# Kernel optimization log

Hardware: AMD Instinct MI355X
Metric: run time of the kernel (lower is better)

The kernel has to match this reference:

```python
import jax, jax.numpy as jnp
import numpy as np
from functools import partial

NUM_HEADS = 8
EPS = 1e-12  # torch F.normalize default eps


def conv1x1(x, w):
    # x: [b,i,h,w], w: [o,i] -> [b,o,h,w]
    return jnp.einsum('oi,bihw->bohw', w, x)


def dwconv3x3(x, w):
    # depthwise 3x3, SAME padding; x: [b,c,h,w], w: [c,1,3,3]
    c = x.shape[1]
    return jax.lax.conv_general_dilated(
        x, w, window_strides=(1, 1), padding='SAME',
        dimension_numbers=('NCHW', 'OIHW', 'NCHW'), feature_group_count=c)


def setup_inputs() -> dict:
    key = jax.random.key(0)
    ks = jax.random.split(key, 16)
    b, dim, h, w = 2, 128, 256, 256
    d8 = dim // 8
    f = lambda k, shape, fan: (jax.random.normal(k, shape, jnp.float32) * (1.0 / np.sqrt(fan)))
    return {
        'x': jax.random.normal(ks[0], (b, dim, h, w), jnp.float32),
        'y': jax.random.normal(ks[1], (b, dim, h, w), jnp.float32),
        'qkv_w': f(ks[2], (dim * 3, dim), dim),
        'qkv_dw_w': f(ks[3], (dim * 3, 1, 3, 3), 9),
        'proj_w': f(ks[4], (dim, dim), dim),
        'sa_w1': f(ks[5], (d8, dim), dim),
        'sa_w2': f(ks[6], (d8, d8), d8),
        'sa_w3': f(ks[7], (1, d8), d8),
        'sp_w1': f(ks[8], (d8, dim), dim),
        'sp_w2': f(ks[9], (d8, d8), d8),
        'sp_w3': f(ks[10], (dim, d8), d8),
        'dw_w': f(ks[11], (dim, 1, 3, 3), 9),
        'temperature': jnp.ones((NUM_HEADS, 1, 1), jnp.float32),
    }


def reference(x, y, qkv_w, qkv_dw_w, proj_w, sa_w1, sa_w2, sa_w3,
              sp_w1, sp_w2, sp_w3, dw_w, temperature):
    b, c, h, w = x.shape
    hd = NUM_HEADS
    # QKV: 1x1 conv then depthwise 3x3
    qkv = dwconv3x3(conv1x1(x, qkv_w), qkv_dw_w)
    q, k, v = jnp.split(qkv, 3, axis=1)
    # Spatial attention gate from y: [b,1,h,w]
    sa = jax.nn.sigmoid(conv1x1(jax.nn.relu(conv1x1(jax.nn.relu(conv1x1(y, sa_w1)), sa_w2)), sa_w3))
    q = q * sa
    # b (head c) h w -> b head c (h w)
    shp = (b, hd, c // hd, h * w)
    q = q.reshape(shp)
    k = k.reshape(shp)
    v = v.reshape(shp)
    # L2 normalize along spatial axis (torch F.normalize semantics)
    q = q / jnp.maximum(jnp.linalg.norm(q, axis=-1, keepdims=True), EPS)
    k = k / jnp.maximum(jnp.linalg.norm(k, axis=-1, keepdims=True), EPS)
    # channel-wise attention: [b,head,c/head,c/head]
    attn = jnp.einsum('bhcn,bhdn->bhcd', q, k) * temperature
    attn = jax.nn.softmax(attn, axis=-1)
    out = jnp.einsum('bhcd,bhdn->bhcn', attn, v).reshape(b, c, h, w)
    # Spectral attention gate from out: [b,c]
    pooled = jnp.mean(out, axis=(2, 3))
    g = jax.nn.gelu(pooled @ sp_w1.T, approximate=False)
    g = jax.nn.gelu(g @ sp_w2.T, approximate=False)
    spec = jax.nn.sigmoid(g @ sp_w3.T)[:, :, None, None]
    y2 = dwconv3x3(y, dw_w) * spec
    return conv1x1(out + y2, proj_w)
```

## Files before the change

kernel.cpp:

```cpp
#include <hip/hip_runtime.h>
#include <hip/hip_bf16.h>

typedef __hip_bfloat16 bf16;
typedef __attribute__((ext_vector_type(8))) short short8;
typedef __attribute__((ext_vector_type(4))) short short4v;
typedef __attribute__((ext_vector_type(4))) int   int4v;
typedef __attribute__((ext_vector_type(4))) float float4v;

#define B_   2
#define C_   128
#define H_   256
#define W_   256
#define HW_  65536
#define HD_  8
#define CH_  16
#define C3_  384
#define NG_  48

static __device__ __forceinline__ float b2f(bf16 v) { return __bfloat162float(v); }
static __device__ __forceinline__ bf16  f2b(float v) { return __float2bfloat16(v); }
static __device__ __forceinline__ short b2s(bf16 v) { return *reinterpret_cast<short*>(&v); }
static __device__ __forceinline__ float su2f(short s) {
  return __uint_as_float(((unsigned)(unsigned short)s) << 16);
}
static __device__ __forceinline__ short f2s(float v) { bf16 h = f2b(v); return b2s(h); }
static __device__ __forceinline__ short8 smask(short8 v, int m) {
  int4v iv = *(int4v*)&v;
  iv = iv & m;
  return *(short8*)&iv;
}

__global__ void k_wprep(const float* __restrict__ qkv_w, const float* __restrict__ proj_w,
                        const float* __restrict__ sa_w1,
                        float* __restrict__ wt_qkvT, float* __restrict__ wt_proj,
                        float* __restrict__ wt_sa1, bf16* __restrict__ wt_qkv_bf,
                        bf16* __restrict__ wt_proj_bf, int do_bf) {
  int idx = blockIdx.x * 256 + threadIdx.x;
  if (idx < C3_ * C_) { int o = idx / C_, i = idx % C_; wt_qkvT[i * C3_ + o] = qkv_w[idx]; }
  if (idx < C_ * C_)  { int o = idx / C_, i = idx % C_; wt_proj[i * C_ + o] = proj_w[idx]; }
  if (idx < 16 * C_)  { int j = idx / C_, i = idx % C_; wt_sa1[i * 16 + j] = sa_w1[idx]; }
  if (do_bf && idx < C3_ * C_) {
    int o = idx / C_, k = idx % C_;
    int sk = ((((k >> 3) ^ (o & 7)) << 3) | (k & 7));
    wt_qkv_bf[o * C_ + sk] = f2b(qkv_w[idx]);
  }
  if (do_bf && idx < C_ * C_) {
    int o = idx / C_, k = idx % C_;
    int sk = ((((k >> 3) ^ (o & 7)) << 3) | (k & 7));
    wt_proj_bf[o * C_ + sk] = f2b(proj_w[idx]);
  }
}

__global__ void __launch_bounds__(256) k_sa(
    const float* __restrict__ y, const float* __restrict__ wt_sa1,
    const float* __restrict__ sa_w2, const float* __restrict__ sa_w3,
    float* __restrict__ sa) {
  int b = blockIdx.y;
  int p0 = (blockIdx.x * 256 + threadIdx.x) * 2;
  const float* yp = y + (size_t)b * C_ * HW_ + p0;
  float t1a[16], t1b[16];
#pragma unroll
  for (int j = 0; j < 16; ++j) { t1a[j] = 0.f; t1b[j] = 0.f; }
  for (int i = 0; i < C_; ++i) {
    float2 v = *(const float2*)(yp + (size_t)i * HW_);
    const float* wr = wt_sa1 + i * 16;
#pragma unroll
    for (int j = 0; j < 16; ++j) { t1a[j] = fmaf(wr[j], v.x, t1a[j]); t1b[j] = fmaf(wr[j], v.y, t1b[j]); }
  }
#pragma unroll
  for (int j = 0; j < 16; ++j) { t1a[j] = fmaxf(t1a[j], 0.f); t1b[j] = fmaxf(t1b[j], 0.f); }
  float t2a[16], t2b[16];
#pragma unroll
  for (int j = 0; j < 16; ++j) {
    float sx = 0.f, sy = 0.f;
#pragma unroll
    for (int l = 0; l < 16; ++l) { float w = sa_w2[j * 16 + l]; sx = fmaf(w, t1a[l], sx); sy = fmaf(w, t1b[l], sy); }
    t2a[j] = fmaxf(sx, 0.f); t2b[j] = fmaxf(sy, 0.f);
  }
  float sa3 = 0.f, sb3 = 0.f;
#pragma unroll
  for (int j = 0; j < 16; ++j) { float w = sa_w3[j]; sa3 = fmaf(w, t2a[j], sa3); sb3 = fmaf(w, t2b[j], sb3); }
  sa[(size_t)b * HW_ + p0]     = 1.f / (1.f + expf(-sa3));
  sa[(size_t)b * HW_ + p0 + 1] = 1.f / (1.f + expf(-sb3));
}

__global__ void __launch_bounds__(256) k_convm(
    const float* __restrict__ x, const bf16* __restrict__ wbf, bf16* __restrict__ pre) {
  __shared__ bf16 XT[2][64][128];
  __shared__ bf16 AT[128][128];
  int b = blockIdx.y;
  int p0 = blockIdx.x * 64;
  int t = threadIdx.x;

  {
    int p  = t & 63;
    int c0 = t >> 6;
    const float* xp = x + (size_t)b * C_ * HW_ + p0 + p;
#pragma unroll
    for (int it = 0; it < 4; ++it) {
      int c = c0 + it * 4;
      short8 hv, lv;
#pragma unroll
      for (int j = 0; j < 8; ++j) {
        float v = xp[(size_t)(c * 8 + j) * HW_];
        bf16 h = f2b(v);
        bf16 l = f2b(v - b2f(h));
        hv[j] = b2s(h); lv[j] = b2s(l);
      }
      int sc = c ^ (p & 7);
      *(short8*)&XT[0][p][sc * 8] = hv;
      *(short8*)&XT[1][p][sc * 8] = lv;
    }
  }

  int lane = t & 63, wave = t >> 6;
  int m = lane & 15, quad = lane >> 4;
  int wr = wave >> 1, wc = wave & 1;
  float4v acc[4][2];

  for (int mb = 0; mb < 3; ++mb) {
    __syncthreads();
    {
      const short8* src = (const short8*)(wbf + mb * C_ * C_);
      short8* dst = (short8*)&AT[0][0];
#pragma unroll
      for (int j = 0; j < 8; ++j)
        dst[j * 256 + t] = src[j * 256 + t];
    }
    __syncthreads();

#pragma unroll
    for (int mt = 0; mt < 4; ++mt)
#pragma unroll
      for (int nt = 0; nt < 2; ++nt)
#pragma unroll
        for (int e = 0; e < 4; ++e) acc[mt][nt][e] = 0.f;

#pragma unroll
    for (int kk = 0; kk < 4; ++kk) {
      int cidx = (((kk * 4 + quad) ^ (m & 7)) << 3);
      short8 af[4], bh[2], bl[2];
#pragma unroll
      for (int mt = 0; mt < 4; ++mt)
        af[mt] = *(const short8*)&AT[wr * 64 + mt * 16 + m][cidx];
#pragma unroll
      for (int nt = 0; nt < 2; ++nt) {
        bh[nt] = *(const short8*)&XT[0][wc * 32 + nt * 16 + m][cidx];
        bl[nt] = *(const short8*)&XT[1][wc * 32 + nt * 16 + m][cidx];
      }
#pragma unroll
      for (int mt = 0; mt < 4; ++mt)
#pragma unroll
        for (int nt = 0; nt < 2; ++nt) {
          acc[mt][nt] = __builtin_amdgcn_mfma_f32_16x16x32_bf16(af[mt], bh[nt], acc[mt][nt], 0, 0, 0);
          acc[mt][nt] = __builtin_amdgcn_mfma_f32_16x16x32_bf16(af[mt], bl[nt], acc[mt][nt], 0, 0, 0);
        }
    }

#pragma unroll
    for (int mt = 0; mt < 4; ++mt)
#pragma unroll
      for (int nt = 0; nt < 2; ++nt) {
        int gl = mb * 16 + wr * 8 + mt * 2 + (quad >> 1);
        int p = wc * 32 + nt * 16 + m;
        short4v sv;
#pragma unroll
        for (int reg = 0; reg < 4; ++reg) sv[reg] = f2s(acc[mt][nt][reg]);
        bf16* dp = pre + (((size_t)b * NG_ + gl) * HW_ + p0 + p) * 8 + (quad & 1) * 4;
        *(short4v*)dp = sv;
      }
  }
}

__global__ void __launch_bounds__(256) k_dwgram(
    const bf16* __restrict__ pre, const float* __restrict__ dww,
    const float* __restrict__ sa, float* __restrict__ attn_raw,
    float* __restrict__ ssq_q, float* __restrict__ ssq_k) {
  __shared__ char smem[65536];
  bf16 (*dwb)[256] = (bf16 (*)[256])(smem + 49152);
  float* red = (float*)smem;

  int b = blockIdx.z, head = blockIdx.y, r0 = blockIdx.x * 8;
  int t = threadIdx.x;
  const float* saw = sa + (size_t)b * HW_;

  int g0 = head * 2;
  size_t gbase0 = (((size_t)b * NG_ + g0)      * HW_) * 8;
  size_t gbase1 = (((size_t)b * NG_ + g0 + 1)  * HW_) * 8;
  size_t gbase2 = (((size_t)b * NG_ + 16 + g0) * HW_) * 8;
  size_t gbase3 = (((size_t)b * NG_ + 17 + g0) * HW_) * 8;

  auto loadrow = [&](int r, int soff) {
    if (r < 0 || r >= H_) {
      short8 z = {0, 0, 0, 0, 0, 0, 0, 0};
      *(short8*)(smem + soff + 0 * 4096 + t * 16) = z;
      *(short8*)(smem + soff + 1 * 4096 + t * 16) = z;
      *(short8*)(smem + soff + 2 * 4096 + t * 16) = z;
      *(short8*)(smem + soff + 3 * 4096 + t * 16) = z;
      return;
    }
    size_t poff = ((size_t)(r * W_ + t)) * 8;
    *(short8*)(smem + soff + 0 * 4096 + t * 16) = *(const short8*)(pre + gbase0 + poff);
    *(short8*)(smem + soff + 1 * 4096 + t * 16) = *(const short8*)(pre + gbase1 + poff);
    *(short8*)(smem + soff + 2 * 4096 + t * 16) = *(const short8*)(pre + gbase2 + poff);
    *(short8*)(smem + soff + 3 * 4096 + t * 16) = *(const short8*)(pre + gbase3 + poff);
  };

  loadrow(r0 - 1, 0); loadrow(r0, 16384); loadrow(r0 + 1, 32768);
  __syncthreads();

  int lane = t & 63, wave = t >> 6;
  int m = lane & 15, quad = lane >> 4;
  int sch = t >> 3;
  int colL = ((t > 0) ? (t - 1) : 0) * 16;
  int colC = t * 16;
  int colR = ((t < W_ - 1) ? (t + 1) : (W_ - 1)) * 16;
  int mskl = (t > 0) ? -1 : 0;
  int mskr = (t < W_ - 1) ? -1 : 0;
  float4v acc = {0.f, 0.f, 0.f, 0.f};
  float sacc = 0.f;

  int so0 = 0, so1 = 16384, so2 = 32768;

  for (int i = 0; i < 8; ++i) {
    int rr = r0 + i;
    short8 q0v, q1v, q2v, q3v;
    bool pf = (i < 7);
    {
      short8 z = {0, 0, 0, 0, 0, 0, 0, 0};
      q0v = z; q1v = z; q2v = z; q3v = z;
    }
    if (pf && (rr + 2) < H_) {
      size_t poff = ((size_t)((rr + 2) * W_ + t)) * 8;
      q0v = *(const short8*)(pre + gbase0 + poff);
      q1v = *(const short8*)(pre + gbase1 + poff);
      q2v = *(const short8*)(pre + gbase2 + poff);
      q3v = *(const short8*)(pre + gbase3 + poff);
    }
    float gate = saw[rr * W_ + t];

    float a[32];
#pragma unroll
    for (int c = 0; c < 32; ++c) a[c] = 0.f;
#pragma unroll
    for (int dy = 0; dy < 3; ++dy) {
      int soff = (dy == 0) ? so0 : ((dy == 1) ? so1 : so2);
#pragma unroll
      for (int cg = 0; cg < 4; ++cg) {
        const char* base = smem + soff + cg * 4096;
        short8 vl = smask(*(const short8*)(base + colL), mskl);
        short8 vc = *(const short8*)(base + colC);
        short8 vr = smask(*(const short8*)(base + colR), mskr);
#pragma unroll
        for (int j = 0; j < 8; ++j) {
          int c = cg * 8 + j;
          int och = (c < 16) ? (head * CH_ + c) : (C_ + head * CH_ + c - 16);
          const float* wp = dww + och * 9 + dy * 3;
          a[c] = fmaf(wp[0], su2f(vl[j]), a[c]);
          a[c] = fmaf(wp[1], su2f(vc[j]), a[c]);
          a[c] = fmaf(wp[2], su2f(vr[j]), a[c]);
        }
      }
    }
#pragma unroll
    for (int c = 0; c < 16; ++c) a[c] *= gate;
#pragma unroll
    for (int c = 0; c < 32; ++c) dwb[c][t ^ ((c & 7) << 3)] = f2b(a[c]);
    __syncthreads();
    if (pf) {
      *(short8*)(smem + so0 + 0 * 4096 + t * 16) = q0v;
      *(short8*)(smem + so0 + 1 * 4096 + t * 16) = q1v;
      *(short8*)(smem + so0 + 2 * 4096 + t * 16) = q2v;
      *(short8*)(smem + so0 + 3 * 4096 + t * 16) = q3v;
    }
#pragma unroll
    for (int cn = 0; cn < 2; ++cn) {
      int p0 = wave * 64 + cn * 32;
      int ca = ((((p0 >> 3) + quad) ^ (m & 7)) << 3);
      short8 af = *(const short8*)&dwb[m][ca];
      short8 bfv = *(const short8*)&dwb[16 + m][ca];
      acc = __builtin_amdgcn_mfma_f32_16x16x32_bf16(af, bfv, acc, 0, 0, 0);
    }
#pragma unroll
    for (int it = 0; it < 4; ++it) {
      int c = (t & 7) + it * 8;
      int cs = c ^ (sch & 7);
      short8 v = *(const short8*)&dwb[sch][cs * 8];
#pragma unroll
      for (int j = 0; j < 8; ++j) { float f = su2f(v[j]); sacc = fmaf(f, f, sacc); }
    }
    __syncthreads();
    int tmp = so0; so0 = so1; so1 = so2; so2 = tmp;
  }

  float* ar = attn_raw + ((size_t)b * HD_ + head) * 256;
#pragma unroll
  for (int reg = 0; reg < 4; ++reg)
    atomicAdd(&ar[(quad * 4 + reg) * 16 + m], acc[reg]);
  red[t] = sacc;
  __syncthreads();
  if (t < 32) {
    float s = 0.f;
#pragma unroll
    for (int k = 0; k < 8; ++k) s += red[t * 8 + k];
    if (t < 16) atomicAdd(&ssq_q[((size_t)b * HD_ + head) * CH_ + t], s);
    else        atomicAdd(&ssq_k[((size_t)b * HD_ + head) * CH_ + t - 16], s);
  }
}

__global__ void k_softmax(const float* __restrict__ attn_raw, const float* __restrict__ ssq_q,
                          const float* __restrict__ ssq_k, const float* __restrict__ temperature,
                          float* __restrict__ attn) {
  int row = threadIdx.x;
  int bh = row >> 4;
  int head = bh & 7;
  float temp = temperature[head];
  float nq = fmaxf(sqrtf(ssq_q[row]), 1e-12f);
  float v[16];
#pragma unroll
  for (int d = 0; d < 16; ++d) {
    float nk = fmaxf(sqrtf(ssq_k[bh * 16 + d]), 1e-12f);
    v[d] = attn_raw[row * 16 + d] / (nq * nk) * temp;
  }
  float m = -1e30f;
#pragma unroll
  for (int d = 0; d < 16; ++d) m = fmaxf(m, v[d]);
  float s = 0.f;
#pragma unroll
  for (int d = 0; d < 16; ++d) { v[d] = expf(v[d] - m); s += v[d]; }
  float inv = 1.f / s;
#pragma unroll
  for (int d = 0; d < 16; ++d) attn[row * 16 + d] = v[d] * inv;
}

__global__ void __launch_bounds__(256) k_out(
    const bf16* __restrict__ pre, const float* __restrict__ dww,
    const float* __restrict__ attn, float* __restrict__ outb,
    float* __restrict__ pooled) {
  __shared__ char smem[24576];
  int b = blockIdx.z, head = blockIdx.y, r0 = blockIdx.x * 4;
  int t = threadIdx.x;

  size_t gbase0 = (((size_t)b * NG_ + 32 + head * 2)     * HW_) * 8;
  size_t gbase1 = (((size_t)b * NG_ + 32 + head * 2 + 1) * HW_) * 8;

  auto loadrow = [&](int r, int soff) {
    if (r < 0 || r >= H_) {
      short8 z = {0, 0, 0, 0, 0, 0, 0, 0};
      *(short8*)(smem + soff + 0 * 4096 + t * 16) = z;
      *(short8*)(smem + soff + 1 * 4096 + t * 16) = z;
      return;
    }
    size_t poff = ((size_t)(r * W_ + t)) * 8;
    *(short8*)(smem + soff + 0 * 4096 + t * 16) = *(const short8*)(pre + gbase0 + poff);
    *(short8*)(smem + soff + 1 * 4096 + t * 16) = *(const short8*)(pre + gbase1 + poff);
  };

  loadrow(r0 - 1, 0); loadrow(r0, 8192); loadrow(r0 + 1, 16384);
  __syncthreads();

  const float* ap = attn + ((size_t)b * HD_ + head) * 256;
  int colL = ((t > 0) ? (t - 1) : 0) * 16;
  int colC = t * 16;
  int colR = ((t < W_ - 1) ? (t + 1) : (W_ - 1)) * 16;
  int mskl = (t > 0) ? -1 : 0;
  int mskr = (t < W_ - 1) ? -1 : 0;
  float psum[16];
#pragma unroll
  for (int c = 0; c < 16; ++c) psum[c] = 0.f;

  int so0 = 0, so1 = 8192, so2 = 16384;

  for (int i = 0; i < 4; ++i) {
    int rr = r0 + i;
    short8 q0v, q1v;
    bool pf = (i < 3);
    {
      short8 z = {0, 0, 0, 0, 0, 0, 0, 0};
      q0v = z; q1v = z;
    }
    if (pf && (rr + 2) < H_) {
      size_t poff = ((size_t)((rr + 2) * W_ + t)) * 8;
      q0v = *(const short8*)(pre + gbase0 + poff);
      q1v = *(const short8*)(pre + gbase1 + poff);
    }

    float vv[16];
#pragma unroll
    for (int c = 0; c < 16; ++c) vv[c] = 0.f;
#pragma unroll
    for (int dy = 0; dy < 3; ++dy) {
      int soff = (dy == 0) ? so0 : ((dy == 1) ? so1 : so2);
#pragma unroll
      for (int cg = 0; cg < 2; ++cg) {
        const char* base = smem + soff + cg * 4096;
        short8 vl = smask(*(const short8*)(base + colL), mskl);
        short8 vc = *(const short8*)(base + colC);
        short8 vr = smask(*(const short8*)(base + colR), mskr);
#pragma unroll
        for (int j = 0; j < 8; ++j) {
          int c = cg * 8 + j;
          const float* wp = dww + (2 * C_ + head * CH_ + c) * 9 + dy * 3;
          vv[c] = fmaf(wp[0], su2f(vl[j]), vv[c]);
          vv[c] = fmaf(wp[1], su2f(vc[j]), vv[c]);
          vv[c] = fmaf(wp[2], su2f(vr[j]), vv[c]);
        }
      }
    }
    float* op = outb + ((size_t)b * C_ + head * CH_) * (size_t)HW_ + rr * W_ + t;
#pragma unroll
    for (int c2 = 0; c2 < 16; ++c2) {
      float s2 = 0.f;
#pragma unroll
      for (int d = 0; d < 16; ++d) s2 = fmaf(ap[c2 * 16 + d], vv[d], s2);
      op[(size_t)c2 * HW_] = s2;
      psum[c2] += s2;
    }
    __syncthreads();
    if (pf) {
      *(short8*)(smem + so0 + 0 * 4096 + t * 16) = q0v;
      *(short8*)(smem + so0 + 1 * 4096 + t * 16) = q1v;
    }
    __syncthreads();
    int tmp = so0; so0 = so1; so1 = so2; so2 = tmp;
  }

  int lane = t & 63;
#pragma unroll
  for (int c = 0; c < 16; ++c) {
#pragma unroll
    for (int off = 32; off > 0; off >>= 1)
      psum[c] += __shfl_xor(psum[c], off, 64);
  }
  if (lane == 0) {
    float* pp = pooled + (size_t)b * C_ + head * CH_;
#pragma unroll
    for (int c = 0; c < 16; ++c) atomicAdd(&pp[c], psum[c]);
  }
}

__global__ void k_pool(const float* __restrict__ outb, float* __restrict__ pooled) {
  int ch = blockIdx.x, b = blockIdx.y;
  const float* p = outb + ((size_t)b * C_ + ch) * (size_t)HW_;
  float s = 0.f;
  for (int i = threadIdx.x * 4; i < HW_; i += 1024) {
    float4 v = *(const float4*)(p + i);
    s += v.x + v.y + v.z + v.w;
  }
#pragma unroll
  for (int off = 32; off > 0; off >>= 1) s += __shfl_down(s, off);
  __shared__ float wsum[4];
  int lane = threadIdx.x & 63, wv = threadIdx.x >> 6;
  if (lane == 0) wsum[wv] = s;
  __syncthreads();
  if (threadIdx.x == 0) {
    float tt = wsum[0] + wsum[1] + wsum[2] + wsum[3];
    pooled[b * C_ + ch] = tt * (1.f / HW_);
  }
}

__global__ void k_spec(const float* __restrict__ pooled, const float* __restrict__ sp_w1,
                       const float* __restrict__ sp_w2, const float* __restrict__ sp_w3,
                       float* __restrict__ spec, float pscale) {
  __shared__ float g1[2][16], g2[2][16];
  int tid = threadIdx.x;
  const float RS2 = 0.70710678118654752f;
  if (tid < 32) {
    int b = tid >> 4, j = tid & 15;
    float s = 0.f;
    for (int i = 0; i < C_; ++i) s = fmaf(sp_w1[j * C_ + i], pooled[b * C_ + i] * pscale, s);
    g1[b][j] = 0.5f * s * (1.f + erff(s * RS2));
  }
  __syncthreads();
  if (tid < 32) {
    int b = tid >> 4, j = tid & 15;
    float s = 0.f;
    for (int l = 0; l < 16; ++l) s = fmaf(sp_w2[j * 16 + l], g1[b][l], s);
    g2[b][j] = 0.5f * s * (1.f + erff(s * RS2));
  }
  __syncthreads();
  {
    int b = tid >> 7, o = tid & 127;
    float s = 0.f;
    for (int jj = 0; jj < 16; ++jj) s = fmaf(sp_w3[o * 16 + jj], g2[b][jj], s);
    spec[b * C_ + o] = 1.f / (1.f + expf(-s));
  }
}

__global__ void __launch_bounds__(256) k_z(
    const float* __restrict__ y, const float* __restrict__ dww,
    const float* __restrict__ spec, float* __restrict__ dout) {
  int b = blockIdx.z, ch = blockIdx.y;
  int row = blockIdx.x * 4 + (threadIdx.x >> 6);
  int c0 = (threadIdx.x & 63) * 4;
  const float* yb = y + ((size_t)b * C_ + ch) * HW_;
  const float* wp = dww + ch * 9;
  float acc[4] = {0.f, 0.f, 0.f, 0.f};
#pragma unroll
  for (int dy = -1; dy <= 1; ++dy) {
    int rrow = row + dy;
    if (rrow < 0 || rrow >= H_) continue;
    const float* yr = yb + rrow * W_;
    float4 cv = *(const float4*)(yr + c0);
    float lf = (c0 > 0) ? yr[c0 - 1] : 0.f;
    float rt = (c0 + 4 < W_) ? yr[c0 + 4] : 0.f;
    float w0 = wp[(dy + 1) * 3], w1 = wp[(dy + 1) * 3 + 1], w2 = wp[(dy + 1) * 3 + 2];
    float v[6] = {lf, cv.x, cv.y, cv.z, cv.w, rt};
#pragma unroll
    for (int j = 0; j < 4; ++j)
      acc[j] = fmaf(w0, v[j], fmaf(w1, v[j + 1], fmaf(w2, v[j + 2], acc[j])));
  }
  float sp = spec[b * C_ + ch];
  float* dp = dout + ((size_t)b * C_ + ch) * HW_ + row * W_ + c0;
  float4 ov = *(const float4*)dp;
  ov.x += acc[0] * sp; ov.y += acc[1] * sp; ov.z += acc[2] * sp; ov.w += acc[3] * sp;
  *(float4*)dp = ov;
}

__global__ void __launch_bounds__(256) k_projm(
    const bf16* __restrict__ wpb, float* __restrict__ dout) {
  __shared__ bf16 XT[2][64][128];
  __shared__ bf16 AT[128][128];
  int b = blockIdx.y;
  int p0 = blockIdx.x * 64;
  int t = threadIdx.x;

  {
    const short8* src = (const short8*)wpb;
    short8* dst = (short8*)&AT[0][0];
#pragma unroll
    for (int j = 0; j < 8; ++j)
      dst[j * 256 + t] = src[j * 256 + t];
  }
  {
    int p  = t & 63;
    int c0 = t >> 6;
    const float* xp = dout + (size_t)b * C_ * HW_ + p0 + p;
#pragma unroll
    for (int it = 0; it < 4; ++it) {
      int c = c0 + it * 4;
      short8 hv, lv;
#pragma unroll
      for (int j = 0; j < 8; ++j) {
        float v = xp[(size_t)(c * 8 + j) * HW_];
        bf16 h = f2b(v);
        bf16 l = f2b(v - b2f(h));
        hv[j] = b2s(h); lv[j] = b2s(l);
      }
      int sc = c ^ (p & 7);
      *(short8*)&XT[0][p][sc * 8] = hv;
      *(short8*)&XT[1][p][sc * 8] = lv;
    }
  }
  __syncthreads();

  int lane = t & 63, wave = t >> 6;
  int m = lane & 15, quad = lane >> 4;
  int wr = wave >> 1, wc = wave & 1;
  float4v acc[4][2];
#pragma unroll
  for (int mt = 0; mt < 4; ++mt)
#pragma unroll
    for (int nt = 0; nt < 2; ++nt)
#pragma unroll
      for (int e = 0; e < 4; ++e) acc[mt][nt][e] = 0.f;

#pragma unroll
  for (int kk = 0; kk < 4; ++kk) {
    int cidx = (((kk * 4 + quad) ^ (m & 7)) << 3);
    short8 af[4], bh[2], bl[2];
#pragma unroll
    for (int mt = 0; mt < 4; ++mt)
      af[mt] = *(const short8*)&AT[wr * 64 + mt * 16 + m][cidx];
#pragma unroll
    for (int nt = 0; nt < 2; ++nt) {
      bh[nt] = *(const short8*)&XT[0][wc * 32 + nt * 16 + m][cidx];
      bl[nt] = *(const short8*)&XT[1][wc * 32 + nt * 16 + m][cidx];
    }
#pragma unroll
    for (int mt = 0; mt < 4; ++mt)
#pragma unroll
      for (int nt = 0; nt < 2; ++nt) {
        acc[mt][nt] = __builtin_amdgcn_mfma_f32_16x16x32_bf16(af[mt], bh[nt], acc[mt][nt], 0, 0, 0);
        acc[mt][nt] = __builtin_amdgcn_mfma_f32_16x16x32_bf16(af[mt], bl[nt], acc[mt][nt], 0, 0, 0);
      }
  }

  float* op = dout + (size_t)b * C_ * HW_ + p0;
#pragma unroll
  for (int mt = 0; mt < 4; ++mt)
#pragma unroll
    for (int nt = 0; nt < 2; ++nt)
#pragma unroll
      for (int reg = 0; reg < 4; ++reg) {
        int o = wr * 64 + mt * 16 + quad * 4 + reg;
        int p = wc * 32 + nt * 16 + m;
        op[(size_t)o * HW_ + p] = acc[mt][nt][reg];
      }
}

__global__ void __launch_bounds__(256) k_gram_fb(
    const float* __restrict__ x, const float* __restrict__ wt_qkvT,
    const float* __restrict__ dww, const float* __restrict__ sa,
    float* __restrict__ attn_raw, float* __restrict__ ssq_q, float* __restrict__ ssq_k) {
  __shared__ bf16 ring[3][32][256];
  __shared__ bf16 dwb[32][256];
  int b = blockIdx.z, head = blockIdx.y, r0 = blockIdx.x * 8;
  int t = threadIdx.x;
  const float* xb = x + (size_t)b * C_ * HW_;
  const float* saw = sa + (size_t)b * HW_;
  auto convrow = [&](int r) {
    int slot = (r + 3) % 3;
    if (r < 0 || r >= H_) {
#pragma unroll
      for (int c = 0; c < 32; ++c) ring[slot][c][t] = f2b(0.f);
      return;
    }
    float acc[32];
#pragma unroll
    for (int c = 0; c < 32; ++c) acc[c] = 0.f;
    const float* xp = xb + r * W_ + t;
    const float* wq = wt_qkvT + head * CH_;
    const float* wk = wt_qkvT + C_ + head * CH_;
    for (int i = 0; i < C_; ++i) {
      float xv = xp[(size_t)i * HW_];
      const float* w1 = wq + i * C3_;
      const float* w2 = wk + i * C3_;
#pragma unroll
      for (int c = 0; c < 16; ++c) acc[c]      = fmaf(w1[c], xv, acc[c]);
#pragma unroll
      for (int c = 0; c < 16; ++c) acc[16 + c] = fmaf(w2[c], xv, acc[16 + c]);
    }
#pragma unroll
    for (int c = 0; c < 32; ++c) ring[slot][c][t] = f2b(acc[c]);
  };
  convrow(r0 - 1); convrow(r0); convrow(r0 + 1);
  __syncthreads();
  int c = t >> 4, d = t & 15;
  float gacc = 0.f, sacc = 0.f;
  for (int rr = r0; rr < r0 + 8; ++rr) {
    float gate = saw[rr * W_ + t];
    for (int ch = 0; ch < 32; ++ch) {
      int och = (ch < 16) ? (head * CH_ + ch) : (C_ + head * CH_ + ch - 16);
      float a = 0.f;
#pragma unroll
      for (int dy = -1; dy <= 1; ++dy) {
        int s = (rr + dy + 3) % 3;
#pragma unroll
        for (int dx = -1; dx <= 1; ++dx) {
          int cc = t + dx;
          if (cc < 0 || cc >= W_) continue;
          a = fmaf(dww[och * 9 + (dy + 1) * 3 + dx + 1], b2f(ring[s][ch][cc]), a);
        }
      }
      if (ch < 16) a *= gate;
      dwb[ch][t] = f2b(a);
    }
    __syncthreads();
    for (int p = 0; p < 256; ++p) {
      int pp = (p + 4 * d + 2 * c) & 255;
      gacc = fmaf(b2f(dwb[c][pp]), b2f(dwb[16 + d][pp]), gacc);
    }
    if (t < 32) {
      for (int p = 0; p < 256; ++p) {
        int pp = (p + 2 * t) & 255;
        float v = b2f(dwb[t][pp]);
        sacc = fmaf(v, v, sacc);
      }
    }
    if (rr < r0 + 7) convrow(rr + 2);
    __syncthreads();
  }
  atomicAdd(&attn_raw[(((size_t)b * HD_ + head) * CH_ + c) * CH_ + d], gacc);
  if (t < 16)      atomicAdd(&ssq_q[((size_t)b * HD_ + head) * CH_ + t], sacc);
  else if (t < 32) atomicAdd(&ssq_k[((size_t)b * HD_ + head) * CH_ + t - 16], sacc);
}

__global__ void __launch_bounds__(256) k_out_fb(
    const float* __restrict__ x, const float* __restrict__ wt_qkvT,
    const float* __restrict__ dww, const float* __restrict__ attn,
    float* __restrict__ outb) {
  __shared__ bf16 ring[3][16][256];
  int b = blockIdx.z, head = blockIdx.y, r0 = blockIdx.x * 8;
  int t = threadIdx.x;
  const float* xb = x + (size_t)b * C_ * HW_;
  auto convrow = [&](int r) {
    int slot = (r + 3) % 3;
    if (r < 0 || r >= H_) {
#pragma unroll
      for (int c = 0; c < 16; ++c) ring[slot][c][t] = f2b(0.f);
      return;
    }
    float acc[16];
#pragma unroll
    for (int c = 0; c < 16; ++c) acc[c] = 0.f;
    const float* xp = xb + r * W_ + t;
    const float* wv = wt_qkvT + 2 * C_ + head * CH_;
    for (int i = 0; i < C_; ++i) {
      float xv = xp[(size_t)i * HW_];
      const float* w1 = wv + i * C3_;
#pragma unroll
      for (int c = 0; c < 16; ++c) acc[c] = fmaf(w1[c], xv, acc[c]);
    }
#pragma unroll
    for (int c = 0; c < 16; ++c) ring[slot][c][t] = f2b(acc[c]);
  };
  convrow(r0 - 1); convrow(r0); convrow(r0 + 1);
  __syncthreads();
  const float* ap = attn + ((size_t)b * HD_ + head) * 256;
  for (int rr = r0; rr < r0 + 8; ++rr) {
    float vv[16];
#pragma unroll
    for (int ch = 0; ch < 16; ++ch) {
      int och = 2 * C_ + head * CH_ + ch;
      float a = 0.f;
#pragma unroll
      for (int dy = -1; dy <= 1; ++dy) {
        int s = (rr + dy + 3) % 3;
#pragma unroll
        for (int dx = -1; dx <= 1; ++dx) {
          int cc = t + dx;
          if (cc < 0 || cc >= W_) continue;
          a = fmaf(dww[och * 9 + (dy + 1) * 3 + dx + 1], b2f(ring[s][ch][cc]), a);
        }
      }
      vv[ch] = a;
    }
    float* op = outb + ((size_t)b * C_ + head * CH_) * (size_t)HW_ + rr * W_ + t;
#pragma unroll
    for (int c2 = 0; c2 < 16; ++c2) {
      float s = 0.f;
#pragma unroll
      for (int d = 0; d < 16; ++d) s = fmaf(ap[c2 * 16 + d], vv[d], s);
      op[(size_t)c2 * HW_] = s;
    }
    __syncthreads();
    if (rr < r0 + 7) convrow(rr + 2);
    __syncthreads();
  }
}

__global__ void __launch_bounds__(256) k_zproj_fb(
    const float* __restrict__ y, const float* __restrict__ dwwz,
    const float* __restrict__ spec, const float* __restrict__ wt_proj,
    float* __restrict__ dout) {
  __shared__ bf16 zt[128][256];
  int b = blockIdx.y, r = blockIdx.x;
  int t = threadIdx.x;
  const float* yb = y + (size_t)b * C_ * HW_;
  float* db = dout + (size_t)b * C_ * HW_;
  for (int ch = 0; ch < C_; ++ch) {
    float a = 0.f;
#pragma unroll
    for (int dy = -1; dy <= 1; ++dy) {
      int hh = r + dy;
      if (hh < 0 || hh >= H_) continue;
      const float* row = yb + (size_t)ch * HW_ + hh * W_;
#pragma unroll
      for (int dx = -1; dx <= 1; ++dx) {
        int cc = t + dx;
        if (cc < 0 || cc >= W_) continue;
        a = fmaf(dwwz[ch * 9 + (dy + 1) * 3 + dx + 1], row[cc], a);
      }
    }
    float z = db[(size_t)ch * HW_ + r * W_ + t] + a * spec[b * C_ + ch];
    zt[ch][t] = f2b(z);
  }
  __syncthreads();
#pragma unroll
  for (int half = 0; half < 2; ++half) {
    float acc[64];
#pragma unroll
    for (int o = 0; o < 64; ++o) acc[o] = 0.f;
    for (int i = 0; i < C_; ++i) {
      float zv = b2f(zt[i][t]);
      const float* wr = wt_proj + i * C_ + half * 64;
#pragma unroll
      for (int o = 0; o < 64; ++o) acc[o] = fmaf(wr[o], zv, acc[o]);
    }
#pragma unroll
    for (int o = 0; o < 64; ++o)
      db[(size_t)(half * 64 + o) * HW_ + r * W_ + t] = acc[o];
  }
}

extern "C" void kernel_launch(void* const* d_in, const int* in_sizes, int n_in,
                              void* d_out, int out_size, void* d_ws, size_t ws_size,
                              hipStream_t stream) {
  const float* x        = (const float*)d_in[0];
  const float* y        = (const float*)d_in[1];
  const float* qkv_w    = (const float*)d_in[2];
  const float* qkv_dw_w = (const float*)d_in[3];
  const float* proj_w   = (const float*)d_in[4];
  const float* sa_w1    = (const float*)d_in[5];
  const float* sa_w2    = (const float*)d_in[6];
  const float* sa_w3    = (const float*)d_in[7];
  const float* sp_w1    = (const float*)d_in[8];
  const float* sp_w2    = (const float*)d_in[9];
  const float* sp_w3    = (const float*)d_in[10];
  const float* dw_w     = (const float*)d_in[11];
  const float* temp     = (const float*)d_in[12];
  float* out = (float*)d_out;

  char* ws = (char*)d_ws;
  float* attn_raw = (float*)(ws + 0);
  float* ssq_q    = (float*)(ws + 16384);
  float* ssq_k    = (float*)(ws + 17408);
  float* attn     = (float*)(ws + 18432);
  float* pooled   = (float*)(ws + 34816);
  float* spec     = (float*)(ws + 35840);
  float* wt_qkvT  = (float*)(ws + 36864);
  float* wt_proj  = (float*)(ws + 233472);
  float* wt_sa1   = (float*)(ws + 299008);
  float* sa       = (float*)(ws + 307200);
  bf16*  wt_qkv_bf = (bf16*)(ws + 835584);
  bf16*  wt_proj_bf= (bf16*)(ws + 933888);
  bf16*  pre      = (bf16*) (ws + 1048576);
  const size_t NEED = 1048576 + 100663296;
  bool big = ws_size >= NEED;

  hipMemsetAsync(ws, 0, 18432, stream);
  hipMemsetAsync(pooled, 0, 1024, stream);

  k_wprep<<<192, 256, 0, stream>>>(qkv_w, proj_w, sa_w1, wt_qkvT, wt_proj, wt_sa1,
                                   wt_qkv_bf, wt_proj_bf, big ? 1 : 0);
  k_sa<<<dim3(HW_ / 512, B_), 256, 0, stream>>>(y, wt_sa1, sa_w2, sa_w3, sa);
  if (big) {
    k_convm<<<dim3(HW_ / 64, B_), 256, 0, stream>>>(x, wt_qkv_bf, pre);
    k_dwgram<<<dim3(H_ / 8, HD_, B_), 256, 0, stream>>>(pre, qkv_dw_w, sa,
                                                        attn_raw, ssq_q, ssq_k);
    k_softmax<<<1, 256, 0, stream>>>(attn_raw, ssq_q, ssq_k, temp, attn);
    k_out<<<dim3(H_ / 4, HD_, B_), 256, 0, stream>>>(pre, qkv_dw_w, attn, out, pooled);
    k_spec<<<1, 256, 0, stream>>>(pooled, sp_w1, sp_w2, sp_w3, spec, 1.f / HW_);
    k_z<<<dim3(H_ / 4, C_, B_), 256, 0, stream>>>(y, dw_w, spec, out);
    k_projm<<<dim3(HW_ / 64, B_), 256, 0, stream>>>(wt_proj_bf, out);
  } else {
    k_gram_fb<<<dim3(H_ / 8, HD_, B_), 256, 0, stream>>>(x, wt_qkvT, qkv_dw_w, sa,
                                                         attn_raw, ssq_q, ssq_k);
    k_softmax<<<1, 256, 0, stream>>>(attn_raw, ssq_q, ssq_k, temp, attn);
    k_out_fb<<<dim3(H_ / 8, HD_, B_), 256, 0, stream>>>(x, wt_qkvT, qkv_dw_w, attn, out);
    k_pool<<<dim3(C_, B_), 256, 0, stream>>>(out, pooled);
    k_spec<<<1, 256, 0, stream>>>(pooled, sp_w1, sp_w2, sp_w3, spec, 1.f);
    k_zproj_fb<<<dim3(H_, B_), 256, 0, stream>>>(y, dw_w, spec, wt_proj, out);
  }
}
```

Baseline: 558.6 us.

## Fuse depthwise y conv and spectral gate into projection GEMM; widen k_out row tiles

Removes the separate k_z pass by computing the depthwise 3x3 conv of y, scaled by the spectral gate, inside the projection kernel's operand load. It then adds this to the attention output before the bf16 hi/lo split. This avoids one full read-modify-write of the 64MB fp32 output buffer. k_out now also processes 8 rows per block instead of 4, which halves the grid and the halo reloads. The cost is 9 scalar, uncoalesced-per-channel y loads per element in the GEMM prologue and fewer blocks for k_out.

```diff
diff --git a/kernel.cpp b/kernel.cpp
--- a/kernel.cpp
+++ b/kernel.cpp
@@ -338,7 +338,7 @@
     const float* __restrict__ attn, float* __restrict__ outb,
     float* __restrict__ pooled) {
   __shared__ char smem[24576];
-  int b = blockIdx.z, head = blockIdx.y, r0 = blockIdx.x * 4;
+  int b = blockIdx.z, head = blockIdx.y, r0 = blockIdx.x * 8;
   int t = threadIdx.x;
 
   size_t gbase0 = (((size_t)b * NG_ + 32 + head * 2)     * HW_) * 8;
@@ -371,10 +371,10 @@
 
   int so0 = 0, so1 = 8192, so2 = 16384;
 
-  for (int i = 0; i < 4; ++i) {
+  for (int i = 0; i < 8; ++i) {
     int rr = r0 + i;
     short8 q0v, q1v;
-    bool pf = (i < 3);
+    bool pf = (i < 7);
     {
       short8 z = {0, 0, 0, 0, 0, 0, 0, 0};
       q0v = z; q1v = z;
@@ -487,38 +487,10 @@
   }
 }
 
-__global__ void __launch_bounds__(256) k_z(
-    const float* __restrict__ y, const float* __restrict__ dww,
-    const float* __restrict__ spec, float* __restrict__ dout) {
-  int b = blockIdx.z, ch = blockIdx.y;
-  int row = blockIdx.x * 4 + (threadIdx.x >> 6);
-  int c0 = (threadIdx.x & 63) * 4;
-  const float* yb = y + ((size_t)b * C_ + ch) * HW_;
-  const float* wp = dww + ch * 9;
-  float acc[4] = {0.f, 0.f, 0.f, 0.f};
-#pragma unroll
-  for (int dy = -1; dy <= 1; ++dy) {
-    int rrow = row + dy;
-    if (rrow < 0 || rrow >= H_) continue;
-    const float* yr = yb + rrow * W_;
-    float4 cv = *(const float4*)(yr + c0);
-    float lf = (c0 > 0) ? yr[c0 - 1] : 0.f;
-    float rt = (c0 + 4 < W_) ? yr[c0 + 4] : 0.f;
-    float w0 = wp[(dy + 1) * 3], w1 = wp[(dy + 1) * 3 + 1], w2 = wp[(dy + 1) * 3 + 2];
-    float v[6] = {lf, cv.x, cv.y, cv.z, cv.w, rt};
-#pragma unroll
-    for (int j = 0; j < 4; ++j)
-      acc[j] = fmaf(w0, v[j], fmaf(w1, v[j + 1], fmaf(w2, v[j + 2], acc[j])));
-  }
-  float sp = spec[b * C_ + ch];
-  float* dp = dout + ((size_t)b * C_ + ch) * HW_ + row * W_ + c0;
-  float4 ov = *(const float4*)dp;
-  ov.x += acc[0] * sp; ov.y += acc[1] * sp; ov.z += acc[2] * sp; ov.w += acc[3] * sp;
-  *(float4*)dp = ov;
-}
-
-__global__ void __launch_bounds__(256) k_projm(
-    const bf16* __restrict__ wpb, float* __restrict__ dout) {
+__global__ void __launch_bounds__(256) k_zprojm(
+    const float* __restrict__ y, const float* __restrict__ dwwz,
+    const float* __restrict__ spec, const bf16* __restrict__ wpb,
+    float* __restrict__ dout) {
   __shared__ bf16 XT[2][64][128];
   __shared__ bf16 AT[128][128];
   int b = blockIdx.y;
@@ -535,17 +507,46 @@
   {
     int p  = t & 63;
     int c0 = t >> 6;
-    const float* xp = dout + (size_t)b * C_ * HW_ + p0 + p;
+    int r  = p0 >> 8;
+    int col = (p0 & 255) + p;
+    const float* dp = dout + (size_t)b * C_ * HW_ + p0 + p;
+    const float* yb = y + (size_t)b * C_ * HW_ + (size_t)r * W_ + col;
+    const float* sb = spec + (size_t)b * C_;
+    bool rTok = (r > 0), rBok = (r < H_ - 1);
+    int loff = (col > 0) ? -1 : 0;
+    int roff = (col < W_ - 1) ? 1 : 0;
+    bool lok = (col > 0), rok = (col < W_ - 1);
 #pragma unroll
     for (int it = 0; it < 4; ++it) {
       int c = c0 + it * 4;
       short8 hv, lv;
 #pragma unroll
       for (int j = 0; j < 8; ++j) {
-        float v = xp[(size_t)(c * 8 + j) * HW_];
-        bf16 h = f2b(v);
-        bf16 l = f2b(v - b2f(h));
-        hv[j] = b2s(h); lv[j] = b2s(l);
+        int ch = c * 8 + j;
+        const float* wp = dwwz + ch * 9;
+        const float* yc = yb + (size_t)ch * HW_;
+        float a = 0.f;
+        if (rTok) {
+          const float* yr = yc - W_;
+          float l = yr[loff]; if (!lok) l = 0.f;
+          float rr2 = yr[roff]; if (!rok) rr2 = 0.f;
+          a = fmaf(wp[0], l, fmaf(wp[1], yr[0], fmaf(wp[2], rr2, a)));
+        }
+        {
+          float l = yc[loff]; if (!lok) l = 0.f;
+          float rr2 = yc[roff]; if (!rok) rr2 = 0.f;
+          a = fmaf(wp[3], l, fmaf(wp[4], yc[0], fmaf(wp[5], rr2, a)));
+        }
+        if (rBok) {
+          const float* yr = yc + W_;
+          float l = yr[loff]; if (!lok) l = 0.f;
+          float rr2 = yr[roff]; if (!rok) rr2 = 0.f;
+          a = fmaf(wp[6], l, fmaf(wp[7], yr[0], fmaf(wp[8], rr2, a)));
+        }
+        float z = dp[(size_t)ch * HW_] + a * sb[ch];
+        bf16 h = f2b(z);
+        hv[j] = b2s(h);
+        lv[j] = b2s(f2b(z - b2f(h)));
       }
       int sc = c ^ (p & 7);
       *(short8*)&XT[0][p][sc * 8] = hv;
@@ -830,10 +831,9 @@
     k_dwgram<<<dim3(H_ / 8, HD_, B_), 256, 0, stream>>>(pre, qkv_dw_w, sa,
                                                         attn_raw, ssq_q, ssq_k);
     k_softmax<<<1, 256, 0, stream>>>(attn_raw, ssq_q, ssq_k, temp, attn);
-    k_out<<<dim3(H_ / 4, HD_, B_), 256, 0, stream>>>(pre, qkv_dw_w, attn, out, pooled);
+    k_out<<<dim3(H_ / 8, HD_, B_), 256, 0, stream>>>(pre, qkv_dw_w, attn, out, pooled);
     k_spec<<<1, 256, 0, stream>>>(pooled, sp_w1, sp_w2, sp_w3, spec, 1.f / HW_);
-    k_z<<<dim3(H_ / 4, C_, B_), 256, 0, stream>>>(y, dw_w, spec, out);
-    k_projm<<<dim3(HW_ / 64, B_), 256, 0, stream>>>(wt_proj_bf, out);
+    k_zprojm<<<dim3(HW_ / 64, B_), 256, 0, stream>>>(y, dw_w, spec, wt_proj_bf, out);
   } else {
     k_gram_fb<<<dim3(H_ / 8, HD_, B_), 256, 0, stream>>>(x, wt_qkvT, qkv_dw_w, sa,
                                                          attn_raw, ssq_q, ssq_k);
```

Result: no change. 568.2 us (+1.7%).
